# Optimization experiments

Hardware: AMD Instinct MI355X
Metric: run time of the kernel (lower is better)

## Reference

```python
import jax, jax.numpy as jnp
import numpy as np

N, CIN, COUT, K, CSTYLE, H, W = 8, 512, 512, 3, 512, 64, 64
EPS = 1e-8
SQRT2 = 2.0 ** 0.5


def setup_inputs() -> dict:
    key = jax.random.key(0)
    ks = jax.random.split(key, 5)
    return {
        "x": jax.random.normal(ks[0], (N, CIN, H, W), jnp.float32),
        "style": jax.random.normal(ks[1], (N, CSTYLE), jnp.float32),
        "noise": jax.random.normal(ks[2], (N, 1, H, W), jnp.float32),
        "conv_weight": jax.random.normal(ks[3], (1, COUT, CIN, K, K), jnp.float32),
        "mod_weight": jax.random.normal(ks[4], (CIN, CSTYLE), jnp.float32) / np.float32(np.sqrt(CSTYLE)),
        "mod_bias": jnp.ones((CIN,), jnp.float32),
        "noise_weight": jnp.zeros((1,), jnp.float32),
        "act_bias": jnp.zeros((COUT,), jnp.float32),
    }


def reference(x, style, noise, conv_weight, mod_weight, mod_bias, noise_weight, act_bias):
    n = x.shape[0]
    # style modulation: linear(style) -> per-sample per-in-channel scale (style_bias=0)
    s = style @ mod_weight.T + mod_bias                       # (n, cin)
    # modulate shared weight (1, cout, cin, k, k) -> (n, cout, cin, k, k)
    w = conv_weight * s[:, None, :, None, None]
    # demodulate
    demod = jax.lax.rsqrt(jnp.sum(w * w, axis=(2, 3, 4)) + EPS)  # (n, cout)
    w = w * demod[:, :, None, None, None]
    # grouped conv: groups = batch
    w = w.reshape(n * COUT, CIN, K, K)
    xg = x.reshape(1, n * CIN, H, W)
    out = jax.lax.conv_general_dilated(
        xg, w,
        window_strides=(1, 1),
        padding=[(K // 2, K // 2), (K // 2, K // 2)],
        dimension_numbers=("NCHW", "OIHW", "NCHW"),
        feature_group_count=n,
    )
    out = out.reshape(n, COUT, H, W) * SQRT2
    # noise injection (scalar weight, broadcast noise)
    out = out + noise_weight[0] * noise
    # fused bias + leaky relu (slope 0.2)
    out = jax.nn.leaky_relu(out + act_bias[None, :, None, None], negative_slope=0.2)
    return out
```

## Files before the change

kernel.cpp:

```cpp
#include <hip/hip_runtime.h>
#include <hip/hip_bf16.h>
#include <stdint.h>


typedef __attribute__((ext_vector_type(8))) short short8;
typedef __attribute__((ext_vector_type(4))) float f32x4;
typedef __attribute__((ext_vector_type(4))) unsigned int uint4v;

__device__ __forceinline__ unsigned short f2bf(float f) {
  unsigned u = __builtin_bit_cast(unsigned, f);
  u += 0x7FFFu + ((u >> 16) & 1u);
  return (unsigned short)(u >> 16);
}

__device__ __forceinline__ void g2l16(const void* g, void* l) {
  __builtin_amdgcn_global_load_lds(
      (const __attribute__((address_space(1))) void*)g,
      (__attribute__((address_space(3))) void*)l, 16, 0, 0);
}

__global__ void k_prep1(const float* __restrict__ style, const float* __restrict__ mw,
                        const float* __restrict__ mb, const float* __restrict__ cw,
                        float* __restrict__ s_out, float* __restrict__ wsq,
                        unsigned short* __restrict__ Wt) {
  __shared__ float ldsf[18432];
  int t = threadIdx.x;
  int b = blockIdx.x;
  if (b < 1024) {
    int wid = b * 4 + (t >> 6);
    int lane = t & 63;
    int n = wid >> 9, ci = wid & 511;
    float sum = 0.f;
#pragma unroll
    for (int i = 0; i < 8; ++i) {
      int k = lane + i * 64;
      sum += style[n * 512 + k] * mw[ci * 512 + k];
    }
#pragma unroll
    for (int off = 32; off; off >>= 1) sum += __shfl_xor(sum, off, 64);
    if (lane == 0) s_out[wid] = sum + mb[ci];
  } else if (b < 2048) {
    int id = (b - 1024) * 256 + t;
    const float* p = cw + (size_t)id * 9;
    float a = 0.f;
#pragma unroll
    for (int j = 0; j < 9; ++j) a += p[j] * p[j];
    wsq[id] = a;
  } else {
    int bb = b - 2048;
    int cb = bb >> 4, kb = bb & 15;
#pragma unroll
    for (int i = 0; i < 72; ++i) {
      int idx = t + i * 256;
      int seg = idx / 288, off = idx - seg * 288;
      ldsf[idx] = cw[(size_t)(cb * 64 + seg) * 4608 + kb * 288 + off];
    }
    __syncthreads();
    unsigned short* ob = Wt + (size_t)(cb * 16 + kb) * 18432;
#pragma unroll
    for (int i = 0; i < 9; ++i) {
      int c = t + i * 256;
      int m = c & 15, lhi = (c >> 4) & 3, mt = (c >> 6) & 3, tap = c >> 8;
      int co_rel = mt * 16 + m;
      unsigned v[8];
#pragma unroll
      for (int j = 0; j < 8; ++j)
        v[j] = f2bf(ldsf[co_rel * 288 + (lhi * 8 + j) * 9 + tap]);
      uint4v o;
      o.x = v[0] | (v[1] << 16);
      o.y = v[2] | (v[3] << 16);
      o.z = v[4] | (v[5] << 16);
      o.w = v[6] | (v[7] << 16);
      *(uint4v*)(ob + (size_t)c * 8) = o;
    }
  }
}

__global__ void k_prep2(const float* __restrict__ s, const float* __restrict__ wsq,
                        const float* __restrict__ x, float* __restrict__ demod,
                        unsigned short* __restrict__ Xp) {
  __shared__ float smem[4225];
  __shared__ float sx[64];
  int t = threadIdx.x;
  int b = blockIdx.x;
  if (b < 1024) {
    int wid = b * 4 + (t >> 6);
    int lane = t & 63;
    int n = wid >> 9, co = wid & 511;
    float sum = 0.f;
#pragma unroll
    for (int i = 0; i < 8; ++i) {
      int ci = lane + i * 64;
      float sv = s[n * 512 + ci];
      sum += sv * sv * wsq[co * 512 + ci];
    }
#pragma unroll
    for (int off = 32; off; off >>= 1) sum += __shfl_xor(sum, off, 64);
    if (lane == 0) demod[wid] = rsqrtf(sum + 1e-8f) * 1.41421356237309515f;
  } else {
    int b2 = b - 1024;
    int cbn = b2 & 7, h = (b2 >> 3) & 63, n = b2 >> 9;
    float(*lds)[65] = (float(*)[65])smem;
    const float* xb = x + (((size_t)n * 512 + cbn * 64) * 64 + h) * 64;
#pragma unroll
    for (int rep = 0; rep < 16; ++rep) {
      int idx = rep * 256 + t;
      int i = idx >> 6, w = idx & 63;
      lds[i][w] = xb[(size_t)i * 4096 + w];
    }
    if (t < 64) sx[t] = s[n * 512 + cbn * 64 + t];
    __syncthreads();
    unsigned short* nb = Xp + (size_t)n * 2230272 + (size_t)(h + 1) * 33792;
#pragma unroll
    for (int rep = 0; rep < 2; ++rep) {
      int c = rep * 256 + t;
      int cig = c >> 6, col = c & 63;
      int kb = cbn * 2 + (cig >> 2), lhi = cig & 3;
      unsigned v[8];
#pragma unroll
      for (int j = 0; j < 8; ++j) v[j] = f2bf(lds[cig * 8 + j][col] * sx[cig * 8 + j]);
      uint4v o;
      o.x = v[0] | (v[1] << 16);
      o.y = v[2] | (v[3] << 16);
      o.z = v[4] | (v[5] << 16);
      o.w = v[6] | (v[7] << 16);
      *(uint4v*)(nb + ((size_t)(kb * 4 + lhi) * 66 + col + 1) * 8) = o;
    }
  }
}

__global__ void __launch_bounds__(256, 2) k_conv(
    const unsigned short* __restrict__ Wt, const unsigned short* __restrict__ Xp,
    const float* __restrict__ demod, const float* __restrict__ noise,
    const float* __restrict__ nw_p, const float* __restrict__ act_bias,
    float* __restrict__ out) {
  __shared__ short lds_a[18432];
  __shared__ short lds_x[22528];
  int t = threadIdx.x;
  int r0 = blockIdx.x * 8;
  int cb = blockIdx.y;
  int n = blockIdx.z;
  int lane = t & 63, wv = t >> 6;
  int l15 = lane & 15, lhi = lane >> 4;

  const unsigned short* abase = Wt + (size_t)cb * 16 * 18432;
  const unsigned short* xbase = Xp + (size_t)n * 2230272;
  int xoffg[11];
#pragma unroll
  for (int j = 0; j < 11; ++j) {
    int c = j * 256 + t;
    int r = c / 264, rc = c - r * 264;
    int off = (r0 + r) * 33792 + rc * 8;
    if (c >= 2640) off = 0;
    xoffg[j] = off;
  }

  f32x4 acc[4][8];
#pragma unroll
  for (int a = 0; a < 4; ++a)
#pragma unroll
    for (int bq = 0; bq < 8; ++bq) acc[a][bq] = (f32x4){0.f, 0.f, 0.f, 0.f};

  const int aoff = lhi * 128 + l15 * 8;
  const int xoffb = lhi * 528 + (wv * 16 + l15) * 8;

  for (int kb = 0; kb < 16; ++kb) {
    __syncthreads();
    const char* ab = (const char*)(abase + (size_t)kb * 18432);
#pragma unroll
    for (int i = 0; i < 9; ++i)
      g2l16(ab + i * 4096 + t * 16, (char*)lds_a + i * 4096 + t * 16);
#pragma unroll
    for (int j = 0; j < 11; ++j)
      g2l16(xbase + xoffg[j] + kb * 2112, (char*)lds_x + j * 4096 + t * 16);
    __syncthreads();

#pragma unroll
    for (int dw = 0; dw < 3; ++dw) {
      short8 bf[10];
#pragma unroll
      for (int rr = 0; rr < 10; ++rr)
        bf[rr] = *(const short8*)(lds_x + rr * 2112 + dw * 8 + xoffb);
#pragma unroll
      for (int dh = 0; dh < 3; ++dh) {
#pragma unroll
        for (int mt = 0; mt < 4; ++mt) {
          short8 af = *(const short8*)(lds_a + (dh * 3 + dw) * 2048 + mt * 512 + aoff);
#pragma unroll
          for (int ri = 0; ri < 8; ++ri)
            acc[mt][ri] =
                __builtin_amdgcn_mfma_f32_16x16x32_bf16(af, bf[ri + dh], acc[mt][ri], 0, 0, 0);
        }
      }
    }
  }

  float nw = nw_p[0];
  int col = wv * 16 + l15;
  float nz[8];
#pragma unroll
  for (int ri = 0; ri < 8; ++ri)
    nz[ri] = nw * noise[((size_t)n * 64 + r0 + ri) * 64 + col];
#pragma unroll
  for (int mt = 0; mt < 4; ++mt) {
    f32x4 dm4 = *(const f32x4*)(demod + n * 512 + cb * 64 + mt * 16 + lhi * 4);
#pragma unroll
    for (int c = 0; c < 4; ++c) {
      int co = cb * 64 + mt * 16 + lhi * 4 + c;
      float ab2 = act_bias[co];
      float dm = dm4[c];
#pragma unroll
      for (int ri = 0; ri < 8; ++ri) {
        float v = dm * acc[mt][ri][c] + nz[ri] + ab2;
        v = v > 0.f ? v : 0.2f * v;
        out[(((size_t)n * 512 + co) * 64 + (r0 + ri)) * 64 + col] = v;
      }
    }
  }
}

extern "C" void kernel_launch(void* const* d_in, const int* in_sizes, int n_in,
                              void* d_out, int out_size, void* d_ws, size_t ws_size,
                              hipStream_t stream) {
  const float* x     = (const float*)d_in[0];
  const float* style = (const float*)d_in[1];
  const float* noise = (const float*)d_in[2];
  const float* cw    = (const float*)d_in[3];
  const float* mw    = (const float*)d_in[4];
  const float* mb    = (const float*)d_in[5];
  const float* nw    = (const float*)d_in[6];
  const float* ab    = (const float*)d_in[7];
  float* out = (float*)d_out;

  char* ws = (char*)d_ws;
  float* s_buf  = (float*)ws;
  float* demod  = (float*)(ws + 16384);
  float* wsq    = (float*)(ws + 32768);
  unsigned short* Wt = (unsigned short*)(ws + 1081344);
  unsigned short* Xp = (unsigned short*)(ws + 5799936);

  hipMemsetAsync(Xp, 0, 35684352, stream);
  k_prep1<<<2176, 256, 0, stream>>>(style, mw, mb, cw, s_buf, wsq, Wt);
  k_prep2<<<5120, 256, 0, stream>>>(s_buf, wsq, x, demod, Xp);
  k_conv<<<dim3(8, 8, 8), 256, 0, stream>>>(Wt, Xp, demod, noise, nw, ab, out);
}
```

Measured before the change: 280.0 us.

## Replace full Xp memset with halo-only zeroing and restructure prep kernels

Drops the 35 MB memset of the padded activation buffer and zeroes only the halo rows and columns inside a new combined mid kernel. The x-transposition blocks now handle a whole row across all 512 channels with float4 loads. The weight transpose moves into the same launch and gets a padded LDS stride to cut bank conflicts. The aim is to cut prep memory traffic and one launch, in exchange for a larger LDS footprint per block and more complex halo indexing that must cover every pad element.

```diff
diff --git a/kernel.cpp b/kernel.cpp
--- a/kernel.cpp
+++ b/kernel.cpp
@@ -6,6 +6,7 @@
 typedef __attribute__((ext_vector_type(8))) short short8;
 typedef __attribute__((ext_vector_type(4))) float f32x4;
 typedef __attribute__((ext_vector_type(4))) unsigned int uint4v;
+typedef __attribute__((ext_vector_type(2))) unsigned int uint2v;
 
 __device__ __forceinline__ unsigned short f2bf(float f) {
   unsigned u = __builtin_bit_cast(unsigned, f);
@@ -19,11 +20,9 @@
       (__attribute__((address_space(3))) void*)l, 16, 0, 0);
 }
 
-__global__ void k_prep1(const float* __restrict__ style, const float* __restrict__ mw,
-                        const float* __restrict__ mb, const float* __restrict__ cw,
-                        float* __restrict__ s_out, float* __restrict__ wsq,
-                        unsigned short* __restrict__ Wt) {
-  __shared__ float ldsf[18432];
+__global__ void k_pre(const float* __restrict__ style, const float* __restrict__ mw,
+                      const float* __restrict__ mb, const float* __restrict__ cw,
+                      float* __restrict__ s_out, float* __restrict__ wsq) {
   int t = threadIdx.x;
   int b = blockIdx.x;
   if (b < 1024) {
@@ -39,21 +38,82 @@
 #pragma unroll
     for (int off = 32; off; off >>= 1) sum += __shfl_xor(sum, off, 64);
     if (lane == 0) s_out[wid] = sum + mb[ci];
-  } else if (b < 2048) {
+  } else {
     int id = (b - 1024) * 256 + t;
     const float* p = cw + (size_t)id * 9;
     float a = 0.f;
 #pragma unroll
     for (int j = 0; j < 9; ++j) a += p[j] * p[j];
     wsq[id] = a;
-  } else {
-    int bb = b - 2048;
+  }
+}
+
+__global__ void k_mid(const float* __restrict__ s, const float* __restrict__ wsq,
+                      const float* __restrict__ x, const float* __restrict__ cw,
+                      float* __restrict__ demod, unsigned short* __restrict__ Xp,
+                      unsigned short* __restrict__ Wt) {
+  __shared__ char smem[74240];
+  int t = threadIdx.x;
+  int b = blockIdx.x;
+  if (b < 512) {
+    int n = b >> 6, h = b & 63;
+    short* ldsx = (short*)smem;
+    float* sxf = (float*)(smem + 69632);
+    sxf[t] = s[n * 512 + t];
+    sxf[t + 256] = s[n * 512 + 256 + t];
+    __syncthreads();
+    const float* xb = x + ((size_t)n * 512) * 4096 + h * 64;
+#pragma unroll
+    for (int i = 0; i < 32; ++i) {
+      int L = t + i * 256;
+      int ci = L >> 4, q = L & 15;
+      f32x4 v = *(const f32x4*)(xb + (size_t)ci * 4096 + q * 4);
+      float sv = sxf[ci];
+      uint2v o;
+      o.x = f2bf(v.x * sv) | ((unsigned)f2bf(v.y * sv) << 16);
+      o.y = f2bf(v.z * sv) | ((unsigned)f2bf(v.w * sv) << 16);
+      *(uint2v*)(ldsx + ci * 68 + q * 4) = o;
+    }
+    __syncthreads();
+    unsigned short* nb = Xp + (size_t)n * 2230272 + (size_t)(h + 1) * 33792;
+#pragma unroll
+    for (int r = 0; r < 16; ++r) {
+      int u = t + r * 256;
+      int cig = u >> 6, col = u & 63;
+      unsigned v[8];
+#pragma unroll
+      for (int j = 0; j < 8; ++j)
+        v[j] = (unsigned short)ldsx[(cig * 8 + j) * 68 + col];
+      uint4v o;
+      o.x = v[0] | (v[1] << 16);
+      o.y = v[2] | (v[3] << 16);
+      o.z = v[4] | (v[5] << 16);
+      o.w = v[6] | (v[7] << 16);
+      *(uint4v*)(nb + ((size_t)cig * 66 + col + 1) * 8) = o;
+    }
+  } else if (b < 1536) {
+    int wid = (b - 512) * 4 + (t >> 6);
+    int lane = t & 63;
+    int n = wid >> 9, co = wid & 511;
+    float sum = 0.f;
+#pragma unroll
+    for (int i = 0; i < 8; ++i) {
+      int ci = lane + i * 64;
+      float sv = s[n * 512 + ci];
+      sum += sv * sv * wsq[co * 512 + ci];
+    }
+#pragma unroll
+    for (int off = 32; off; off >>= 1) sum += __shfl_xor(sum, off, 64);
+    if (lane == 0) demod[wid] = rsqrtf(sum + 1e-8f) * 1.41421356237309515f;
+  } else if (b < 1664) {
+    int bb = b - 1536;
     int cb = bb >> 4, kb = bb & 15;
+    float* ldsf = (float*)smem;
 #pragma unroll
     for (int i = 0; i < 72; ++i) {
       int idx = t + i * 256;
       int seg = idx / 288, off = idx - seg * 288;
-      ldsf[idx] = cw[(size_t)(cb * 64 + seg) * 4608 + kb * 288 + off];
+      ldsf[seg * 289 + off] = cw[(size_t)(cb * 64 + seg) * 4608 + kb * 288 + off];
     }
     __syncthreads();
     unsigned short* ob = Wt + (size_t)(cb * 16 + kb) * 18432;
@@ -65,7 +125,7 @@
       unsigned v[8];
 #pragma unroll
       for (int j = 0; j < 8; ++j)
-        v[j] = f2bf(ldsf[co_rel * 288 + (lhi * 8 + j) * 9 + tap]);
+        v[j] = f2bf(ldsf[co_rel * 289 + (lhi * 8 + j) * 9 + tap]);
       uint4v o;
       o.x = v[0] | (v[1] << 16);
       o.y = v[2] | (v[3] << 16);
@@ -73,58 +133,30 @@
       o.w = v[6] | (v[7] << 16);
       *(uint4v*)(ob + (size_t)c * 8) = o;
     }
-  }
-}
-
-__global__ void k_prep2(const float* __restrict__ s, const float* __restrict__ wsq,
-                        const float* __restrict__ x, float* __restrict__ demod,
-                        unsigned short* __restrict__ Xp) {
-  __shared__ float smem[4225];
-  __shared__ float sx[64];
-  int t = threadIdx.x;
-  int b = blockIdx.x;
-  if (b < 1024) {
-    int wid = b * 4 + (t >> 6);
-    int lane = t & 63;
-    int n = wid >> 9, co = wid & 511;
-    float sum = 0.f;
-#pragma unroll
-    for (int i = 0; i < 8; ++i) {
-      int ci = lane + i * 64;
-      float sv = s[n * 512 + ci];
-      sum += sv * sv * wsq[co * 512 + ci];
-    }
-#pragma unroll
-    for (int off = 32; off; off >>= 1) sum += __shfl_xor(sum, off, 64);
-    if (lane == 0) demod[wid] = rsqrtf(sum + 1e-8f) * 1.41421356237309515f;
   } else {
-    int b2 = b - 1024;
-    int cbn = b2 & 7, h = (b2 >> 3) & 63, n = b2 >> 9;
-    float(*lds)[65] = (float(*)[65])smem;
-    const float* xb = x + (((size_t)n * 512 + cbn * 64) * 64 + h) * 64;
-#pragma unroll
-    for (int rep = 0; rep < 16; ++rep) {
-      int idx = rep * 256 + t;
-      int i = idx >> 6, w = idx & 63;
-      lds[i][w] = xb[(size_t)i * 4096 + w];
-    }
-    if (t < 64) sx[t] = s[n * 512 + cbn * 64 + t];
-    __syncthreads();
-    unsigned short* nb = Xp + (size_t)n * 2230272 + (size_t)(h + 1) * 33792;
-#pragma unroll
-    for (int rep = 0; rep < 2; ++rep) {
-      int c = rep * 256 + t;
-      int cig = c >> 6, col = c & 63;
-      int kb = cbn * 2 + (cig >> 2), lhi = cig & 3;
-      unsigned v[8];
-#pragma unroll
-      for (int j = 0; j < 8; ++j) v[j] = f2bf(lds[cig * 8 + j][col] * sx[cig * 8 + j]);
-      uint4v o;
-      o.x = v[0] | (v[1] << 16);
-      o.y = v[2] | (v[3] << 16);
-      o.z = v[4] | (v[5] << 16);
-      o.w = v[6] | (v[7] << 16);
-      *(uint4v*)(nb + ((size_t)(kb * 4 + lhi) * 66 + col + 1) * 8) = o;
+    int bb = b - 1664;
+    int n = bb / 17, part = bb % 17;
+    uint4v z = (uint4v){0u, 0u, 0u, 0u};
+    unsigned short* base = Xp + (size_t)n * 2230272;
+#pragma unroll
+    for (int i = 0; i < 4; ++i) {
+      int id = part * 1024 + i * 256 + t;
+      if (id < 16640) {
+        size_t off;
+        if (id < 8448) {
+          int row = (id < 4224) ? 0 : 65;
+          int c = id - ((id < 4224) ? 0 : 4224);
+          off = (size_t)row * 33792 + (size_t)c * 8;
+        } else {
+          int id2 = id - 8448;
+          int row = 1 + (id2 >> 7);
+          int rem = id2 & 127;
+          int klhi = rem >> 1;
+          int col = (rem & 1) ? 65 : 0;
+          off = (size_t)row * 33792 + ((size_t)klhi * 66 + col) * 8;
+        }
+        *(uint4v*)(base + off) = z;
+      }
     }
   }
 }
@@ -239,8 +271,7 @@
   unsigned short* Wt = (unsigned short*)(ws + 1081344);
   unsigned short* Xp = (unsigned short*)(ws + 5799936);
 
-  hipMemsetAsync(Xp, 0, 35684352, stream);
-  k_prep1<<<2176, 256, 0, stream>>>(style, mw, mb, cw, s_buf, wsq, Wt);
-  k_prep2<<<5120, 256, 0, stream>>>(s_buf, wsq, x, demod, Xp);
+  k_pre<<<2048, 256, 0, stream>>>(style, mw, mb, cw, s_buf, wsq);
+  k_mid<<<1800, 256, 0, stream>>>(s_buf, wsq, x, cw, demod, Xp, Wt);
   k_conv<<<dim3(8, 8, 8), 256, 0, stream>>>(Wt, Xp, demod, noise, nw, ab, out);
 }
```

After: 273.0 us. -2.5%, faster.
